# Optimization experiments

Measured on AMD Instinct MI355X. Metric: run time of the kernel, lower is better.

The kernel has to match this reference:

```python
import jax, jax.numpy as jnp
import numpy as np

B, K, T, C = 4, 8, 2048, 64

def setup_inputs() -> dict:
    key = jax.random.key(0)
    ks = jax.random.split(key, 7)
    return {
        "x": jax.random.normal(ks[0], (B, K, T, C), dtype=jnp.float32),
        "Wq": jax.random.normal(ks[1], (C, C), dtype=jnp.float32) / np.sqrt(C),
        "bq": jax.random.normal(ks[2], (C,), dtype=jnp.float32) * 0.01,
        "Wk": jax.random.normal(ks[3], (C, C), dtype=jnp.float32) / np.sqrt(C),
        "bk": jax.random.normal(ks[4], (C,), dtype=jnp.float32) * 0.01,
        "Wv": jax.random.normal(ks[5], (C, C), dtype=jnp.float32) / np.sqrt(C),
        "bv": jax.random.normal(ks[6], (C,), dtype=jnp.float32) * 0.01,
    }

def reference(x, Wq, bq, Wk, bk, Wv, bv):
    c_dim = x.shape[-1]
    # torch nn.Linear: y = x @ W.T + b
    q = jnp.einsum('bktc,dc->bktd', x, Wq) + bq
    k = jnp.einsum('bktc,dc->bktd', x, Wk) + bk
    v = jnp.einsum('bktc,dc->bktd', x, Wv) + bv
    scores = jnp.einsum('bkic,bkjc->bkij', q, k) / jnp.sqrt(jnp.float32(c_dim))
    attn = jax.nn.softmax(scores, axis=-1)
    out = jnp.einsum('bkij,bkjc->bkic', attn, v)
    return out
```

## Files before the change

kernel.cpp:

```cpp
#include <hip/hip_runtime.h>


#define T_DIM 2048
#define NHEAD 32
#define HSTRIDE (T_DIM * 64)
#define QSCALE 0.18033688011112042f
#define SOFF  8.0f

#define SWZ(row, grp) ((row) * 64 + ((((grp) ^ ((row) & 7)) & 7) * 8))

#define RAW_BARRIER() asm volatile("s_waitcnt lgkmcnt(0)\n\ts_barrier" ::: "memory")

typedef _Float16 h8 __attribute__((ext_vector_type(8)));
typedef _Float16 h4 __attribute__((ext_vector_type(4)));
typedef __fp16   g2 __attribute__((ext_vector_type(2)));
typedef float    f4 __attribute__((ext_vector_type(4)));
typedef float    fv16 __attribute__((ext_vector_type(16)));

union H4U { h4 v; g2 p[2]; };
union H8U { h8 v; h4 h[2]; g2 p[4]; };

#if defined(__has_builtin)
#if __has_builtin(__builtin_amdgcn_exp2f)
#define EXP2(x) __builtin_amdgcn_exp2f(x)
#endif
#endif
#ifndef EXP2
__device__ inline float exp2_raw(float x) {
    float r;
    asm("v_exp_f32 %0, %1" : "=v"(r) : "v"(x));
    return r;
}
#define EXP2(x) exp2_raw(x)
#endif

__device__ inline h4 cvt4(f4 x) {
    H4U u;
    u.p[0] = __builtin_amdgcn_cvt_pkrtz(x[0], x[1]);
    u.p[1] = __builtin_amdgcn_cvt_pkrtz(x[2], x[3]);
    return u.v;
}

__device__ inline h8 cvt8(f4 a, f4 b) {
    H8U r;
    r.h[0] = cvt4(a);
    r.h[1] = cvt4(b);
    return r.v;
}

__device__ inline fv16 splat16(float x) {
    fv16 r;
    #pragma unroll
    for (int i = 0; i < 16; ++i) r[i] = x;
    return r;
}

__global__ __launch_bounds__(256) void qkv_proj_kernel(
    const float* __restrict__ x,
    const float* __restrict__ Wq, const float* __restrict__ bq,
    const float* __restrict__ Wk, const float* __restrict__ bk,
    const float* __restrict__ Wv, const float* __restrict__ bv,
    _Float16* __restrict__ qh, _Float16* __restrict__ khT,
    _Float16* __restrict__ vtT)
{
    __shared__ _Float16 ws[3][64 * 64];
    __shared__ _Float16 ot[64 * 64];
    __shared__ float bsh[3][64];

    const int tid  = threadIdx.x;
    const int row0 = blockIdx.x * 64;
    const int head = blockIdx.x >> 5;
    const int t0   = (blockIdx.x & 31) * 64;

    #pragma unroll
    for (int m = 0; m < 3; ++m) {
        const float* Wm = (m == 0) ? Wq : ((m == 1) ? Wk : Wv);
        const float* bm = (m == 0) ? bq : ((m == 1) ? bk : bv);
        #pragma unroll
        for (int pass = 0; pass < 4; ++pass) {
            const int idx = pass * 1024 + tid * 4;
            const int d = idx >> 6, c = idx & 63;
            f4 wv = *(const f4*)(Wm + idx);
            *(h4*)&ws[m][SWZ(d, c >> 3) + (c & 7)] = cvt4(wv);
        }
        if (tid < 64) bsh[m][tid] = bm[tid];
    }

    const int w    = tid >> 6;
    const int lane = tid & 63;
    const int l15  = lane & 15;
    const int qd   = lane >> 4;

    h8 af[2];
    {
        const float* xp = x + (size_t)(row0 + w * 16 + l15) * 64 + qd * 8;
        #pragma unroll
        for (int ch = 0; ch < 2; ++ch) {
            f4 a0 = *(const f4*)(xp + ch * 32);
            f4 a1 = *(const f4*)(xp + ch * 32 + 4);
            af[ch] = cvt8(a0, a1);
        }
    }
    __syncthreads();

    #pragma unroll
    for (int m = 0; m < 3; ++m) {
        h8 bf[4][2];
        #pragma unroll
        for (int ns = 0; ns < 4; ++ns)
            #pragma unroll
            for (int ch = 0; ch < 2; ++ch)
                bf[ns][ch] = *(const h8*)&ws[m][SWZ(ns * 16 + l15, ch * 4 + qd)];

        f4 acc[4];
        #pragma unroll
        for (int ns = 0; ns < 4; ++ns)
            acc[ns] = (f4){0.f, 0.f, 0.f, 0.f};
        #pragma unroll
        for (int ch = 0; ch < 2; ++ch)
            #pragma unroll
            for (int ns = 0; ns < 4; ++ns)
                acc[ns] = __builtin_amdgcn_mfma_f32_16x16x32_f16(
                    af[ch], bf[ns][ch], acc[ns], 0, 0, 0);

        __syncthreads();
        if (m < 2) {
            #pragma unroll
            for (int ns = 0; ns < 4; ++ns) {
                const int d = ns * 16 + l15;
                const float bias = bsh[m][d];
                #pragma unroll
                for (int r = 0; r < 4; ++r) {
                    const int t = w * 16 + qd * 4 + r;
                    float v = acc[ns][r] + bias;
                    if (m == 0) v *= QSCALE;
                    ot[SWZ(t, d >> 3) + (d & 7)] = (_Float16)v;
                }
            }
            __syncthreads();
            if (m == 0) {
                #pragma unroll
                for (int pass = 0; pass < 2; ++pass) {
                    const int t  = pass * 32 + (tid >> 3);
                    const int c0 = (tid & 7) * 8;
                    *(h8*)&qh[(size_t)(row0 + t) * 64 + c0] =
                        *(const h8*)&ot[SWZ(t, tid & 7)];
                }
            } else {
                #pragma unroll
                for (int pass = 0; pass < 2; ++pass) {
                    const int f   = pass * 2048 + tid * 8;
                    const int kb  = f >> 11;
                    const int cs  = (f >> 9) & 3;
                    const int l   = (f >> 3) & 63;
                    const int p   = l & 31;
                    const int w16 = p & 15;
                    const int sw  = ((w16 & 12) == 4) ? (w16 + 4)
                                  : (((w16 & 12) == 8) ? (w16 - 4) : w16);
                    const int tact = kb * 32 + (p & 16) + sw;
                    const int g8   = cs * 2 + (l >> 5);
                    *(h8*)&khT[(size_t)head * HSTRIDE + (t0 >> 6) * 4096 + f] =
                        *(const h8*)&ot[SWZ(tact, g8)];
                }
            }
        } else {
            #pragma unroll
            for (int ns = 0; ns < 4; ++ns) {
                const int d = ns * 16 + l15;
                const float bias = bsh[2][d];
                const int tl = w * 16 + qd * 4;
                f4 pvf;
                #pragma unroll
                for (int r = 0; r < 4; ++r)
                    pvf[r] = acc[ns][r] + bias;
                *(h4*)&ot[SWZ(d, tl >> 3) + (tl & 7)] = cvt4(pvf);
            }
            __syncthreads();
            #pragma unroll
            for (int pass = 0; pass < 2; ++pass) {
                const int f  = pass * 2048 + tid * 8;
                const int q2 = f >> 9;
                const int b  = q2 >> 1, cc = q2 & 1;
                const int l  = (f >> 3) & 63;
                const int c  = cc * 32 + (l & 31);
                const int tg = b * 2 + (l >> 5);
                *(h8*)&vtT[(size_t)head * HSTRIDE + (t0 >> 6) * 4096 + f] =
                    *(const h8*)&ot[SWZ(c, tg)];
            }
        }
    }
}

__global__ __launch_bounds__(384, 3) void attn_kernel(
    const _Float16* __restrict__ qh, const _Float16* __restrict__ khT,
    const _Float16* __restrict__ vtT, float* __restrict__ out)
{
    __shared__ _Float16 tiles[2][8192];
    const int tid  = threadIdx.x;
    const int w    = tid >> 6;
    const int lane = tid & 63;

    const int bid  = blockIdx.x;
    const int xcd  = bid & 7;
    const int slot = bid >> 3;
    const int head = xcd * 4 + (slot >> 4);
    const int qpart = slot & 15;

    if (w < 4) {
        const int q0  = qpart * 128 + w * 32;
        const int l31 = lane & 31;
        const int lh  = lane >> 5;

        h8 qf[4];
        {
            const _Float16* qp = qh + (size_t)(head * T_DIM + q0 + l31) * 64 + lh * 8;
            #pragma unroll
            for (int cs = 0; cs < 4; ++cs)
                qf[cs] = *(const h8*)(qp + cs * 16);
        }

        f4 rs4 = (f4){0.f, 0.f, 0.f, 0.f};
        fv16 oacc[2];
        oacc[0] = splat16(0.f);
        oacc[1] = splat16(0.f);

        const int ko = lane * 8;
        __syncthreads();

        for (int it = 0; it < 32; ++it) {
            const _Float16* kb_ = &tiles[it & 1][0];
            const _Float16* vb_ = kb_ + 4096;

            fv16 st[2];
            #pragma unroll
            for (int kb = 0; kb < 2; ++kb) {
                h8 kf[4];
                #pragma unroll
                for (int cs = 0; cs < 4; ++cs)
                    kf[cs] = *(const h8*)(kb_ + kb * 2048 + cs * 512 + ko);
                st[kb] = splat16(-SOFF);
                #pragma unroll
                for (int cs = 0; cs < 4; ++cs)
                    st[kb] = __builtin_amdgcn_mfma_f32_32x32x16_f16(
                        kf[cs], qf[cs], st[kb], 0, 0, 0);
            }

            h8 vf[4][2];
            #pragma unroll
            for (int b = 0; b < 4; ++b)
                #pragma unroll
                for (int cc = 0; cc < 2; ++cc)
                    vf[b][cc] = *(const h8*)(vb_ + (b * 2 + cc) * 512 + ko);

            H8U pa[4];
            #pragma unroll
            for (int kb = 0; kb < 2; ++kb)
                #pragma unroll
                for (int g = 0; g < 4; ++g) {
                    f4 p;
                    p[0] = EXP2(st[kb][4 * g + 0]);
                    p[1] = EXP2(st[kb][4 * g + 1]);
                    p[2] = EXP2(st[kb][4 * g + 2]);
                    p[3] = EXP2(st[kb][4 * g + 3]);
                    rs4 += p;
                    const int b = kb * 2 + (g >> 1);
                    pa[b].p[(g & 1) * 2 + 0] = __builtin_amdgcn_cvt_pkrtz(p[0], p[1]);
                    pa[b].p[(g & 1) * 2 + 1] = __builtin_amdgcn_cvt_pkrtz(p[2], p[3]);
                }

            #pragma unroll
            for (int b = 0; b < 4; ++b)
                #pragma unroll
                for (int cc = 0; cc < 2; ++cc)
                    oacc[cc] = __builtin_amdgcn_mfma_f32_32x32x16_f16(
                        pa[b].v, vf[b][cc], oacc[cc], 0, 0, 0);

            __syncthreads();
        }

        float lsum = (rs4[0] + rs4[1]) + (rs4[2] + rs4[3]);
        lsum += __shfl_xor(lsum, 32, 64);
        const float linv = 1.f / lsum;
        #pragma unroll
        for (int r = 0; r < 16; ++r) {
            const int qrow = (r & 3) + 8 * (r >> 2) + 4 * lh;
            const float fac = __shfl(linv, qrow, 64);
            #pragma unroll
            for (int cc = 0; cc < 2; ++cc)
                out[(size_t)(head * T_DIM + q0 + qrow) * 64 + cc * 32 + l31] =
                    oacc[cc][r] * fac;
        }
    } else {
        const _Float16* src = ((w == 4) ? khT : vtT) + (size_t)head * HSTRIDE;
        _Float16* d0 = &tiles[0][(w - 4) * 4096];
        _Float16* d1 = &tiles[1][(w - 4) * 4096];
        const int lo = lane * 8;
        h8 sA[8], sB[8];
        #pragma unroll
        for (int b = 0; b < 8; ++b) sA[b] = *(const h8*)(src + b * 512 + lo);
        #pragma unroll
        for (int b = 0; b < 8; ++b) sB[b] = *(const h8*)(src + 4096 + b * 512 + lo);
        const _Float16* sp = src + 8192;
        #pragma unroll
        for (int b = 0; b < 8; ++b) *(h8*)(d0 + b * 512 + lo) = sA[b];
        RAW_BARRIER();

        for (int it2 = 0; it2 < 16; ++it2) {
            if (it2 < 15) {
                #pragma unroll
                for (int b = 0; b < 8; ++b) sA[b] = *(const h8*)(sp + b * 512 + lo);
                sp += 4096;
            }
            #pragma unroll
            for (int b = 0; b < 8; ++b) *(h8*)(d1 + b * 512 + lo) = sB[b];
            RAW_BARRIER();
            if (it2 < 15) {
                #pragma unroll
                for (int b = 0; b < 8; ++b) sB[b] = *(const h8*)(sp + b * 512 + lo);
                sp += 4096;
                #pragma unroll
                for (int b = 0; b < 8; ++b) *(h8*)(d0 + b * 512 + lo) = sA[b];
            }
            RAW_BARRIER();
        }
    }
}

extern "C" void kernel_launch(void* const* d_in, const int* in_sizes, int n_in,
                              void* d_out, int out_size, void* d_ws, size_t ws_size,
                              hipStream_t stream)
{
    (void)in_sizes; (void)n_in; (void)out_size; (void)ws_size;
    const float* x  = (const float*)d_in[0];
    const float* Wq = (const float*)d_in[1];
    const float* bq = (const float*)d_in[2];
    const float* Wk = (const float*)d_in[3];
    const float* bk = (const float*)d_in[4];
    const float* Wv = (const float*)d_in[5];
    const float* bv = (const float*)d_in[6];
    float* out = (float*)d_out;

    _Float16* qh  = (_Float16*)d_ws;
    _Float16* khT = qh + (size_t)NHEAD * HSTRIDE;
    _Float16* vtT = khT + (size_t)NHEAD * HSTRIDE;

    hipLaunchKernelGGL(qkv_proj_kernel, dim3(1024), dim3(256), 0, stream,
                       x, Wq, bq, Wk, bk, Wv, bv, qh, khT, vtT);
    hipLaunchKernelGGL(attn_kernel, dim3(512), dim3(384), 0, stream,
                       qh, khT, vtT, out);
}
```

Measured before the change: 127.9 us.

## Double query rows per wave and software-pipeline QK with triple-buffered K/V tiles

Each compute wave now handles 64 query rows instead of 32, which halves the grid to 256 blocks and halves K/V tile reloads per query. LDS grows to three K/V tile buffers, and the QK^T MFMAs for the next tile are issued after the PV MFMAs of the current tile so score computation overlaps softmax and PV work. The producer waves are reworked to fill a rotating three-buffer ring. The cost is more registers (occupancy hint lowered to 2) and fewer blocks than the 256 CUs can absorb well.

```diff
diff --git a/kernel.cpp b/kernel.cpp
--- a/kernel.cpp
+++ b/kernel.cpp
@@ -191,11 +191,11 @@
     }
 }
 
-__global__ __launch_bounds__(384, 3) void attn_kernel(
+__global__ __launch_bounds__(384, 2) void attn_kernel(
     const _Float16* __restrict__ qh, const _Float16* __restrict__ khT,
     const _Float16* __restrict__ vtT, float* __restrict__ out)
 {
-    __shared__ _Float16 tiles[2][8192];
+    __shared__ _Float16 tiles[3][8192];
     const int tid  = threadIdx.x;
     const int w    = tid >> 6;
     const int lane = tid & 63;
@@ -203,125 +203,184 @@
     const int bid  = blockIdx.x;
     const int xcd  = bid & 7;
     const int slot = bid >> 3;
-    const int head = xcd * 4 + (slot >> 4);
-    const int qpart = slot & 15;
+    const int head = xcd * 4 + (slot >> 3);
+    const int qpart = slot & 7;
 
     if (w < 4) {
-        const int q0  = qpart * 128 + w * 32;
+        const int q0  = qpart * 256 + w * 64;
         const int l31 = lane & 31;
         const int lh  = lane >> 5;
 
-        h8 qf[4];
+        h8 qf[2][4];
+        #pragma unroll
+        for (int qs = 0; qs < 2; ++qs) {
+            const _Float16* qp = qh + (size_t)(head * T_DIM + q0 + qs * 32 + l31) * 64 + lh * 8;
+            #pragma unroll
+            for (int cs = 0; cs < 4; ++cs)
+                qf[qs][cs] = *(const h8*)(qp + cs * 16);
+        }
+
+        f4 rs4[2] = {(f4){0.f,0.f,0.f,0.f}, (f4){0.f,0.f,0.f,0.f}};
+        fv16 oacc[2][2];
+        #pragma unroll
+        for (int qs = 0; qs < 2; ++qs)
+            #pragma unroll
+            for (int cc = 0; cc < 2; ++cc)
+                oacc[qs][cc] = splat16(0.f);
+
+        const int ko = lane * 8;
+        const _Float16* c0 = &tiles[0][0];
+        const _Float16* c1 = &tiles[1][0];
+        const _Float16* c2 = &tiles[2][0];
+
+        __syncthreads();
+
+        fv16 st[2][2];
         {
-            const _Float16* qp = qh + (size_t)(head * T_DIM + q0 + l31) * 64 + lh * 8;
+            h8 kf[2][4];
+            #pragma unroll
+            for (int kb = 0; kb < 2; ++kb)
+                #pragma unroll
+                for (int cs = 0; cs < 4; ++cs)
+                    kf[kb][cs] = *(const h8*)(c0 + kb * 2048 + cs * 512 + ko);
+            #pragma unroll
+            for (int kb = 0; kb < 2; ++kb)
+                #pragma unroll
+                for (int qs = 0; qs < 2; ++qs)
+                    st[kb][qs] = splat16(-SOFF);
             #pragma unroll
             for (int cs = 0; cs < 4; ++cs)
-                qf[cs] = *(const h8*)(qp + cs * 16);
-        }
-
-        f4 rs4 = (f4){0.f, 0.f, 0.f, 0.f};
-        fv16 oacc[2];
-        oacc[0] = splat16(0.f);
-        oacc[1] = splat16(0.f);
-
-        const int ko = lane * 8;
-        __syncthreads();
+                #pragma unroll
+                for (int kb = 0; kb < 2; ++kb)
+                    #pragma unroll
+                    for (int qs = 0; qs < 2; ++qs)
+                        st[kb][qs] = __builtin_amdgcn_mfma_f32_32x32x16_f16(
+                            kf[kb][cs], qf[qs][cs], st[kb][qs], 0, 0, 0);
+        }
 
         for (int it = 0; it < 32; ++it) {
-            const _Float16* kb_ = &tiles[it & 1][0];
-            const _Float16* vb_ = kb_ + 4096;
-
-            fv16 st[2];
-            #pragma unroll
-            for (int kb = 0; kb < 2; ++kb) {
-                h8 kf[4];
+            h8 kf[2][4];
+            if (it < 31) {
+                #pragma unroll
+                for (int kb = 0; kb < 2; ++kb)
+                    #pragma unroll
+                    for (int cs = 0; cs < 4; ++cs)
+                        kf[kb][cs] = *(const h8*)(c1 + kb * 2048 + cs * 512 + ko);
+            }
+            h8 vf[4][2];
+            #pragma unroll
+            for (int b = 0; b < 4; ++b)
+                #pragma unroll
+                for (int cc = 0; cc < 2; ++cc)
+                    vf[b][cc] = *(const h8*)(c0 + 4096 + (b * 2 + cc) * 512 + ko);
+
+            #pragma unroll
+            for (int qs = 0; qs < 2; ++qs) {
+                H8U pa[4];
+                #pragma unroll
+                for (int kb = 0; kb < 2; ++kb)
+                    #pragma unroll
+                    for (int g = 0; g < 4; ++g) {
+                        f4 p;
+                        p[0] = EXP2(st[kb][qs][4 * g + 0]);
+                        p[1] = EXP2(st[kb][qs][4 * g + 1]);
+                        p[2] = EXP2(st[kb][qs][4 * g + 2]);
+                        p[3] = EXP2(st[kb][qs][4 * g + 3]);
+                        rs4[qs] += p;
+                        const int b = kb * 2 + (g >> 1);
+                        pa[b].p[(g & 1) * 2 + 0] = __builtin_amdgcn_cvt_pkrtz(p[0], p[1]);
+                        pa[b].p[(g & 1) * 2 + 1] = __builtin_amdgcn_cvt_pkrtz(p[2], p[3]);
+                    }
+                #pragma unroll
+                for (int b = 0; b < 4; ++b)
+                    #pragma unroll
+                    for (int cc = 0; cc < 2; ++cc)
+                        oacc[qs][cc] = __builtin_amdgcn_mfma_f32_32x32x16_f16(
+                            pa[b].v, vf[b][cc], oacc[qs][cc], 0, 0, 0);
+            }
+
+            if (it < 31) {
+                #pragma unroll
+                for (int kb = 0; kb < 2; ++kb)
+                    #pragma unroll
+                    for (int qs = 0; qs < 2; ++qs)
+                        st[kb][qs] = splat16(-SOFF);
                 #pragma unroll
                 for (int cs = 0; cs < 4; ++cs)
-                    kf[cs] = *(const h8*)(kb_ + kb * 2048 + cs * 512 + ko);
-                st[kb] = splat16(-SOFF);
-                #pragma unroll
-                for (int cs = 0; cs < 4; ++cs)
-                    st[kb] = __builtin_amdgcn_mfma_f32_32x32x16_f16(
-                        kf[cs], qf[cs], st[kb], 0, 0, 0);
-            }
-
-            h8 vf[4][2];
-            #pragma unroll
-            for (int b = 0; b < 4; ++b)
+                    #pragma unroll
+                    for (int kb = 0; kb < 2; ++kb)
+                        #pragma unroll
+                        for (int qs = 0; qs < 2; ++qs)
+                            st[kb][qs] = __builtin_amdgcn_mfma_f32_32x32x16_f16(
+                                kf[kb][cs], qf[qs][cs], st[kb][qs], 0, 0, 0);
+            }
+
+            const _Float16* tmp = c0; c0 = c1; c1 = c2; c2 = tmp;
+            __syncthreads();
+        }
+
+        #pragma unroll
+        for (int qs = 0; qs < 2; ++qs) {
+            float lsum = (rs4[qs][0] + rs4[qs][1]) + (rs4[qs][2] + rs4[qs][3]);
+            lsum += __shfl_xor(lsum, 32, 64);
+            const float linv = 1.f / lsum;
+            #pragma unroll
+            for (int r = 0; r < 16; ++r) {
+                const int qrow = (r & 3) + 8 * (r >> 2) + 4 * lh;
+                const float fac = __shfl(linv, qrow, 64);
                 #pragma unroll
                 for (int cc = 0; cc < 2; ++cc)
-                    vf[b][cc] = *(const h8*)(vb_ + (b * 2 + cc) * 512 + ko);
-
-            H8U pa[4];
-            #pragma unroll
-            for (int kb = 0; kb < 2; ++kb)
-                #pragma unroll
-                for (int g = 0; g < 4; ++g) {
-                    f4 p;
-                    p[0] = EXP2(st[kb][4 * g + 0]);
-                    p[1] = EXP2(st[kb][4 * g + 1]);
-                    p[2] = EXP2(st[kb][4 * g + 2]);
-                    p[3] = EXP2(st[kb][4 * g + 3]);
-                    rs4 += p;
-                    const int b = kb * 2 + (g >> 1);
-                    pa[b].p[(g & 1) * 2 + 0] = __builtin_amdgcn_cvt_pkrtz(p[0], p[1]);
-                    pa[b].p[(g & 1) * 2 + 1] = __builtin_amdgcn_cvt_pkrtz(p[2], p[3]);
-                }
-
-            #pragma unroll
-            for (int b = 0; b < 4; ++b)
-                #pragma unroll
-                for (int cc = 0; cc < 2; ++cc)
-                    oacc[cc] = __builtin_amdgcn_mfma_f32_32x32x16_f16(
-                        pa[b].v, vf[b][cc], oacc[cc], 0, 0, 0);
-
-            __syncthreads();
-        }
-
-        float lsum = (rs4[0] + rs4[1]) + (rs4[2] + rs4[3]);
-        lsum += __shfl_xor(lsum, 32, 64);
-        const float linv = 1.f / lsum;
-        #pragma unroll
-        for (int r = 0; r < 16; ++r) {
-            const int qrow = (r & 3) + 8 * (r >> 2) + 4 * lh;
-            const float fac = __shfl(linv, qrow, 64);
-            #pragma unroll
-            for (int cc = 0; cc < 2; ++cc)
-                out[(size_t)(head * T_DIM + q0 + qrow) * 64 + cc * 32 + l31] =
-                    oacc[cc][r] * fac;
+                    out[(size_t)(head * T_DIM + q0 + qs * 32 + qrow) * 64 + cc * 32 + l31] =
+                        oacc[qs][cc][r] * fac;
+            }
         }
     } else {
         const _Float16* src = ((w == 4) ? khT : vtT) + (size_t)head * HSTRIDE;
-        _Float16* d0 = &tiles[0][(w - 4) * 4096];
-        _Float16* d1 = &tiles[1][(w - 4) * 4096];
+        const int off = (w - 4) * 4096;
+        _Float16* d0 = &tiles[0][off];
+        _Float16* d1 = &tiles[1][off];
+        _Float16* d2 = &tiles[2][off];
         const int lo = lane * 8;
         h8 sA[8], sB[8];
+
         #pragma unroll
         for (int b = 0; b < 8; ++b) sA[b] = *(const h8*)(src + b * 512 + lo);
         #pragma unroll
         for (int b = 0; b < 8; ++b) sB[b] = *(const h8*)(src + 4096 + b * 512 + lo);
-        const _Float16* sp = src + 8192;
         #pragma unroll
         for (int b = 0; b < 8; ++b) *(h8*)(d0 + b * 512 + lo) = sA[b];
+        #pragma unroll
+        for (int b = 0; b < 8; ++b) *(h8*)(d1 + b * 512 + lo) = sB[b];
+        #pragma unroll
+        for (int b = 0; b < 8; ++b) sA[b] = *(const h8*)(src + 8192 + b * 512 + lo);
+        const _Float16* sp = src + 3 * 4096;
         RAW_BARRIER();
 
-        for (int it2 = 0; it2 < 16; ++it2) {
-            if (it2 < 15) {
+        _Float16* w0 = d2;
+        _Float16* w1 = d0;
+        _Float16* w2 = d1;
+
+        for (int t2 = 0; t2 < 16; ++t2) {
+            if (t2 < 15) {
+                #pragma unroll
+                for (int b = 0; b < 8; ++b) sB[b] = *(const h8*)(sp + b * 512 + lo);
+                sp += 4096;
+                #pragma unroll
+                for (int b = 0; b < 8; ++b) *(h8*)(w0 + b * 512 + lo) = sA[b];
+            }
+            RAW_BARRIER();
+            { _Float16* t = w0; w0 = w1; w1 = w2; w2 = t; }
+            if (t2 < 14) {
                 #pragma unroll
                 for (int b = 0; b < 8; ++b) sA[b] = *(const h8*)(sp + b * 512 + lo);
                 sp += 4096;
             }
-            #pragma unroll
-            for (int b = 0; b < 8; ++b) *(h8*)(d1 + b * 512 + lo) = sB[b];
+            if (t2 < 15) {
+                #pragma unroll
+                for (int b = 0; b < 8; ++b) *(h8*)(w0 + b * 512 + lo) = sB[b];
+            }
             RAW_BARRIER();
-            if (it2 < 15) {
-                #pragma unroll
-                for (int b = 0; b < 8; ++b) sB[b] = *(const h8*)(sp + b * 512 + lo);
-                sp += 4096;
-                #pragma unroll
-                for (int b = 0; b < 8; ++b) *(h8*)(d0 + b * 512 + lo) = sA[b];
-            }
-            RAW_BARRIER();
+            { _Float16* t = w0; w0 = w1; w1 = w2; w2 = t; }
         }
     }
 }
@@ -346,6 +405,6 @@
 
     hipLaunchKernelGGL(qkv_proj_kernel, dim3(1024), dim3(256), 0, stream,
                        x, Wq, bq, Wk, bk, Wv, bv, qh, khT, vtT);
-    hipLaunchKernelGGL(attn_kernel, dim3(512), dim3(384), 0, stream,
+    hipLaunchKernelGGL(attn_kernel, dim3(256), dim3(384), 0, stream,
                        qh, khT, vtT, out);
 }
```

Result: faster. 124.9 us (-2.4%).
